# Kernel optimization log

Measured on AMD Instinct MI355X. Metric: run time of the kernel, lower is better.

Reference implementation:

```python
import jax, jax.numpy as jnp
import numpy as np

K = 9            # LCN box-filter size
EPS = 1e-6


def _box_sum(x):
    """9x9 box sum with zero padding 4, separable. x: [N,H,W] -> [N,H,W]."""
    xp = x[:, None]                                  # N,1,H,W
    kh = jnp.ones((1, 1, K, 1), x.dtype)
    kw = jnp.ones((1, 1, 1, K), x.dtype)
    y = jax.lax.conv_general_dilated(xp, kh, (1, 1), [(K // 2, K // 2), (0, 0)])
    y = jax.lax.conv_general_dilated(y, kw, (1, 1), [(0, 0), (K // 2, K // 2)])
    return y[:, 0]


def _lcn(img):
    """Faithful to torch: conv weight is ones(3,3,9,9)/81, i.e. the 'mean' SUMS over
    the 3 input channels of per-pixel 9x9 box means; every output channel is identical.
    So compute channel-sum once, box-filter it, and broadcast back over channels."""
    kk = float(K * K)
    mean_local = _box_sum(img.sum(axis=1)) / kk                 # N,H,W
    mean_sq_local = _box_sum((img * img).sum(axis=1)) / kk      # N,H,W
    std_local = (mean_sq_local - mean_local * mean_local) * kk / (kk - 1.0)
    m = mean_local[:, None]                                     # N,1,H,W (broadcasts over C)
    s = std_local[:, None]
    return (img - m) / (s + EPS), m, s


def _warp(right, disp):
    """Equivalent of affine_grid(identity) + grid -= (disp*2/W, 0) + grid_sample
    (bilinear, zeros padding, align_corners=False). Since the y-coordinate is the
    identity grid, iy == row index exactly, so sampling reduces to 1-D horizontal
    bilinear interpolation at source column ix = j - disp[n,i,j]."""
    N, C, H, W = right.shape
    ix = jnp.arange(W, dtype=right.dtype)[None, None, :] - disp   # N,H,W
    x0 = jnp.floor(ix)
    wx = ix - x0                                                  # frac weight for x1
    x0i = x0.astype(jnp.int32)
    x1i = x0i + 1
    v0 = ((x0i >= 0) & (x0i < W)).astype(right.dtype)             # zeros padding masks
    v1 = ((x1i >= 0) & (x1i < W)).astype(right.dtype)
    i0 = jnp.broadcast_to(jnp.clip(x0i, 0, W - 1)[:, None], right.shape)
    i1 = jnp.broadcast_to(jnp.clip(x1i, 0, W - 1)[:, None], right.shape)
    g0 = jnp.take_along_axis(right, i0, axis=3)                   # N,C,H,W
    g1 = jnp.take_along_axis(right, i1, axis=3)
    return g0 * (v0 * (1.0 - wx))[:, None] + g1 * (v1 * wx)[:, None]


def setup_inputs() -> dict:
    key = jax.random.key(0)
    k1, k2, k3 = jax.random.split(key, 3)
    N, C, H, W = 8, 3, 720, 1280
    left_img = jax.random.uniform(k1, (N, C, H, W), dtype=jnp.float32)
    right_img = jax.random.uniform(k2, (N, C, H, W), dtype=jnp.float32)
    dispmap = jax.random.uniform(k3, (N, H, W), dtype=jnp.float32) * 64.0  # pixels
    return {"left_img": left_img, "right_img": right_img, "dispmap": dispmap}


def reference(left_img, right_img, dispmap):
    recon_img = _warp(right_img, dispmap)
    recon_img_lcn, _, _ = _lcn(recon_img)
    left_img_lcn, _, left_std_local = _lcn(left_img)
    return jnp.abs((left_img_lcn - recon_img_lcn) * left_std_local).mean()
```

## Files before the change

### kernel.cpp

```cpp
#include <hip/hip_runtime.h>

#define NB 8
#define CC 3
#define HH 720
#define WW 1280
#define EPSL 1e-6f
#define HSEG 30
#define NSEG (HH / HSEG)
#define G4   (NSEG / 4)
#define OUTC 56
#define NSTRIP 23
#define NITER (HSEG + 8)
#define NBLK (NB * NSTRIP * G4)

__device__ __forceinline__ float bperm(int addr, float x) {
    return __int_as_float(__builtin_amdgcn_ds_bpermute(addr, __float_as_int(x)));
}

__global__ __launch_bounds__(256)
void fused_loss_kernel(const float* __restrict__ left,
                       const float* __restrict__ right,
                       const float* __restrict__ disp,
                       float* __restrict__ out)
{
    const int t    = threadIdx.x;
    const int lane = t & 63;
    const int wid  = t >> 6;

    const int b     = blockIdx.x;
    const int strip = b % NSTRIP;
    const int g     = (b / NSTRIP) % G4;
    const int n     = b / (NSTRIP * G4);

    const int hseg = g * 4 + wid;
    const int h0   = hseg * HSEG;

    const int gc  = strip * OUTC + lane - 4;
    const int gcc = min(max(gc, 0), WW - 1);
    const float gcf = (float)gc;
    const bool col_ok   = (gc >= 0) && (gc < WW);
    const bool out_lane = (lane >= 4) && (lane < 4 + OUTC) && (gc < WW);

    const size_t plane = (size_t)HH * WW;
    const float* __restrict__ dp  = disp  + (size_t)n * plane;
    const float* __restrict__ lp0 = left  + (size_t)n * CC * plane;
    const float* __restrict__ lp1 = lp0 + plane;
    const float* __restrict__ lp2 = lp1 + plane;
    const float* __restrict__ rp0 = right + (size_t)n * CC * plane;
    const float* __restrict__ rp1 = rp0 + plane;
    const float* __restrict__ rp2 = rp1 + plane;

    const int a_m1 = ((lane + 63) & 63) << 2;
    const int a_p1 = ((lane +  1) & 63) << 2;
    const int a_m3 = ((lane + 61) & 63) << 2;
    const int a_p3 = ((lane +  3) & 63) << 2;

    __shared__ float4 ring[8][256];

    float p1l0=0,p1l1=0,p1l2=0,p1r0=0,p1r1=0,p1r2=0;
    float p2l0=0,p2l1=0,p2l2=0,p2r0=0,p2r1=0,p2r2=0;
    float p3l0=0,p3l1=0,p3l2=0,p3r0=0,p3r1=0,p3r2=0;
    float p4l0=0,p4l1=0,p4l2=0,p4r0=0,p4r1=0,p4r2=0;

    const int r0 = h0 - 4;

    int rcl = min(max(r0, 0), HH - 1);
    unsigned ro = (unsigned)(rcl * WW + gcc);
    float dA  = dp[ro];
    float al0 = lp0[ro], al1 = lp1[ro], al2 = lp2[ro];
    rcl = min(max(r0 + 1, 0), HH - 1);
    unsigned rob = (unsigned)(rcl * WW + gcc);
    float dB  = dp[rob];
    float bl0 = lp0[rob], bl1 = lp1[rob], bl2 = lp2[rob];

    float aw0, aw1, ag00, ag01, ag10, ag11, ag20, ag21;
    {
        float ix  = gcf - dA;
        float x0f = floorf(ix), wx = ix - x0f;
        int x0i = (int)x0f, x1i = x0i + 1;
        float v0 = (x0i >= 0 && x0i < WW) ? 1.f : 0.f;
        float v1 = (x1i >= 0 && x1i < WW) ? 1.f : 0.f;
        int i0 = min(max(x0i, 0), WW - 1), i1 = min(max(x1i, 0), WW - 1);
        aw0 = v0 * (1.f - wx); aw1 = v1 * wx;
        unsigned rb = (unsigned)(min(max(r0, 0), HH - 1) * WW);
        ag00 = rp0[rb + i0]; ag01 = rp0[rb + i1];
        ag10 = rp1[rb + i0]; ag11 = rp1[rb + i1];
        ag20 = rp2[rb + i0]; ag21 = rp2[rb + i1];
    }

    float4 vsum = make_float4(0.f,0.f,0.f,0.f);
    float acc = 0.f;

    for (int iter = 0; iter < NITER; ++iter) {
        const int r = r0 + iter;

        float4 old8 = ring[iter & 7][t];

        int rcl2 = min(max(r + 2, 0), HH - 1);
        unsigned ro2 = (unsigned)(rcl2 * WW + gcc);
        float dC  = dp[ro2];
        float cl0 = lp0[ro2], cl1 = lp1[ro2], cl2 = lp2[ro2];

        float bw0, bw1, bg00, bg01, bg10, bg11, bg20, bg21;
        {
            float ix  = gcf - dB;
            float x0f = floorf(ix), wx = ix - x0f;
            int x0i = (int)x0f, x1i = x0i + 1;
            float v0 = (x0i >= 0 && x0i < WW) ? 1.f : 0.f;
            float v1 = (x1i >= 0 && x1i < WW) ? 1.f : 0.f;
            int i0 = min(max(x0i, 0), WW - 1), i1 = min(max(x1i, 0), WW - 1);
            bw0 = v0 * (1.f - wx); bw1 = v1 * wx;
            unsigned rb = (unsigned)(min(max(r + 1, 0), HH - 1) * WW);
            bg00 = rp0[rb + i0]; bg01 = rp0[rb + i1];
            bg10 = rp1[rb + i0]; bg11 = rp1[rb + i1];
            bg20 = rp2[rb + i0]; bg21 = rp2[rb + i1];
        }

        float rca = ag00*aw0 + ag01*aw1;
        float rcb = ag10*aw0 + ag11*aw1;
        float rcc = ag20*aw0 + ag21*aw1;
        bool valr = col_ok && ((unsigned)r < (unsigned)HH);
        float rx = al0 + al1 + al2;
        float ry = al0*al0 + al1*al1 + al2*al2;
        float rz = rca + rcb + rcc;
        float rw = rca*rca + rcb*rcb + rcc*rcc;
        rx = valr ? rx : 0.f;  ry = valr ? ry : 0.f;
        rz = valr ? rz : 0.f;  rw = valr ? rw : 0.f;

        float sx = bperm(a_m1, rx) + rx + bperm(a_p1, rx);
        float sy = bperm(a_m1, ry) + ry + bperm(a_p1, ry);
        float sz = bperm(a_m1, rz) + rz + bperm(a_p1, rz);
        float sw = bperm(a_m1, rw) + rw + bperm(a_p1, rw);
        float hx = bperm(a_m3, sx) + sx + bperm(a_p3, sx);
        float hy = bperm(a_m3, sy) + sy + bperm(a_p3, sy);
        float hz = bperm(a_m3, sz) + sz + bperm(a_p3, sz);
        float hw = bperm(a_m3, sw) + sw + bperm(a_p3, sw);

        ring[iter & 7][t] = make_float4(hx, hy, hz, hw);

        vsum.x += hx; vsum.y += hy; vsum.z += hz; vsum.w += hw;

        if (iter >= 8) {
            float ml   = vsum.x * (1.f / 81.f);
            float msl  = vsum.y * (1.f / 81.f);
            float stdl = (msl - ml * ml) * (81.f / 80.f);
            float sl   = stdl + EPSL;
            float invl = __builtin_amdgcn_rcpf(sl);
            invl = invl * __builtin_fmaf(-sl, invl, 2.f);
            float mr   = vsum.z * (1.f / 81.f);
            float msr  = vsum.w * (1.f / 81.f);
            float stdr = (msr - mr * mr) * (81.f / 80.f);
            float sr   = stdr + EPSL;
            float invr = __builtin_amdgcn_rcpf(sr);
            invr = invr * __builtin_fmaf(-sr, invr, 2.f);
            if (out_lane) {
                float av, bv;
                av = (p4l0 - ml) * invl; bv = (p4r0 - mr) * invr;
                acc += fabsf((av - bv) * stdl);
                av = (p4l1 - ml) * invl; bv = (p4r1 - mr) * invr;
                acc += fabsf((av - bv) * stdl);
                av = (p4l2 - ml) * invl; bv = (p4r2 - mr) * invr;
                acc += fabsf((av - bv) * stdl);
            }
            vsum.x -= old8.x; vsum.y -= old8.y; vsum.z -= old8.z; vsum.w -= old8.w;
        }

        p4l0=p3l0; p4l1=p3l1; p4l2=p3l2; p4r0=p3r0; p4r1=p3r1; p4r2=p3r2;
        p3l0=p2l0; p3l1=p2l1; p3l2=p2l2; p3r0=p2r0; p3r1=p2r1; p3r2=p2r2;
        p2l0=p1l0; p2l1=p1l1; p2l2=p1l2; p2r0=p1r0; p2r1=p1r1; p2r2=p1r2;
        p1l0=al0;  p1l1=al1;  p1l2=al2;  p1r0=rca;  p1r1=rcb;  p1r2=rcc;

        al0=bl0; al1=bl1; al2=bl2;
        aw0=bw0; aw1=bw1;
        ag00=bg00; ag01=bg01; ag10=bg10; ag11=bg11; ag20=bg20; ag21=bg21;
        dB=dC; bl0=cl0; bl1=cl1; bl2=cl2;
    }

#pragma unroll
    for (int off = 32; off > 0; off >>= 1)
        acc += __shfl_down(acc, off, 64);
    __syncthreads();
    float* red = (float*)&ring[0][0];
    if (lane == 0) red[wid] = acc;
    __syncthreads();
    if (t == 0) {
        float s = red[0] + red[1] + red[2] + red[3];
        const float inv_count = 1.f / ((float)NB * CC * HH * WW);
        atomicAdd(out, s * inv_count);
    }
}

extern "C" void kernel_launch(void* const* d_in, const int* in_sizes, int n_in,
                              void* d_out, int out_size, void* d_ws, size_t ws_size,
                              hipStream_t stream) {
    const float* left  = (const float*)d_in[0];
    const float* right = (const float*)d_in[1];
    const float* disp  = (const float*)d_in[2];
    float* out = (float*)d_out;

    hipMemsetAsync(out, 0, sizeof(float) * out_size, stream);

    hipLaunchKernelGGL(fused_loss_kernel, dim3(NBLK), dim3(256), 0, stream,
                       left, right, disp, out);
}
```

Before: 244.6 us.

## Process two rows per iteration and reload left pixels instead of shifting registers

The row loop now handles two image rows per step, with deeper software prefetch of disparity, left and gathered right values (two rows ahead). The 4-deep register shift chain of left and recon values is replaced: left center pixels are re-read from global memory (likely cached) at output time, and only the recon values are kept in a 2-stage pair chain. The ring buffer is split into two 4-slot rings. The aim is more memory-level parallelism and fewer register moves per row, at the cost of extra global loads, higher register pressure and possible occupancy loss.

```diff
diff --git a/kernel.cpp b/kernel.cpp
--- a/kernel.cpp
+++ b/kernel.cpp
@@ -10,8 +10,45 @@
 #define G4   (NSEG / 4)
 #define OUTC 56
 #define NSTRIP 23
-#define NITER (HSEG + 8)
+#define NST  ((HSEG + 8) / 2)
 #define NBLK (NB * NSTRIP * G4)
+
+#define OFFR(row) ((unsigned)(min(max((row),0),HH-1)*WW + gcc))
+
+#define GATHER(row, dv, w0_, w1_, g00_, g01_, g10_, g11_, g20_, g21_) do { \
+    float ix_ = gcf - (dv); float x0f_ = floorf(ix_); float wx_ = ix_ - x0f_; \
+    int x0i_ = (int)x0f_; int x1i_ = x0i_ + 1;                              \
+    float v0_ = (x0i_ >= 0 && x0i_ < WW) ? 1.f : 0.f;                       \
+    float v1_ = (x1i_ >= 0 && x1i_ < WW) ? 1.f : 0.f;                       \
+    int i0_ = min(max(x0i_,0),WW-1); int i1_ = min(max(x1i_,0),WW-1);       \
+    w0_ = v0_*(1.f-wx_); w1_ = v1_*wx_;                                     \
+    unsigned rb_ = (unsigned)(min(max((row),0),HH-1)*WW);                   \
+    g00_ = rp0[rb_+i0_]; g01_ = rp0[rb_+i1_];                               \
+    g10_ = rp1[rb_+i0_]; g11_ = rp1[rb_+i1_];                               \
+    g20_ = rp2[rb_+i0_]; g21_ = rp2[rb_+i1_]; } while(0)
+
+#define OUTROW(pa,pb,pc, la,lb,lc) do {                                      \
+    float ml_  = vsum.x*(1.f/81.f);                                          \
+    float msl_ = vsum.y*(1.f/81.f);                                          \
+    float stdl_=(msl_-ml_*ml_)*(81.f/80.f);                                  \
+    float sl_=stdl_+EPSL;                                                    \
+    float invl_=__builtin_amdgcn_rcpf(sl_);                                  \
+    invl_ = invl_*__builtin_fmaf(-sl_,invl_,2.f);                            \
+    float mr_  = vsum.z*(1.f/81.f);                                          \
+    float msr_ = vsum.w*(1.f/81.f);                                          \
+    float stdr_=(msr_-mr_*mr_)*(81.f/80.f);                                  \
+    float sr_=stdr_+EPSL;                                                    \
+    float invr_=__builtin_amdgcn_rcpf(sr_);                                  \
+    invr_ = invr_*__builtin_fmaf(-sr_,invr_,2.f);                            \
+    if (out_lane) {                                                          \
+        float av_,bv_;                                                       \
+        av_=((la)-ml_)*invl_; bv_=((pa)-mr_)*invr_;                          \
+        acc += fabsf((av_-bv_)*stdl_);                                       \
+        av_=((lb)-ml_)*invl_; bv_=((pb)-mr_)*invr_;                          \
+        acc += fabsf((av_-bv_)*stdl_);                                       \
+        av_=((lc)-ml_)*invl_; bv_=((pc)-mr_)*invr_;                          \
+        acc += fabsf((av_-bv_)*stdl_);                                       \
+    } } while(0)
 
 __device__ __forceinline__ float bperm(int addr, float x) {
     return __int_as_float(__builtin_amdgcn_ds_bpermute(addr, __float_as_int(x)));
@@ -32,9 +69,7 @@
     const int g     = (b / NSTRIP) % G4;
     const int n     = b / (NSTRIP * G4);
 
-    const int hseg = g * 4 + wid;
-    const int h0   = hseg * HSEG;
-
+    const int h0 = (g * 4 + wid) * HSEG;
     const int gc  = strip * OUTC + lane - 4;
     const int gcc = min(max(gc, 0), WW - 1);
     const float gcf = (float)gc;
@@ -55,132 +90,114 @@
     const int a_m3 = ((lane + 61) & 63) << 2;
     const int a_p3 = ((lane +  3) & 63) << 2;
 
-    __shared__ float4 ring[8][256];
-
-    float p1l0=0,p1l1=0,p1l2=0,p1r0=0,p1r1=0,p1r2=0;
-    float p2l0=0,p2l1=0,p2l2=0,p2r0=0,p2r1=0,p2r2=0;
-    float p3l0=0,p3l1=0,p3l2=0,p3r0=0,p3r1=0,p3r2=0;
-    float p4l0=0,p4l1=0,p4l2=0,p4r0=0,p4r1=0,p4r2=0;
+    __shared__ float4 ringA[4][256];
+    __shared__ float4 ringB[4][256];
 
     const int r0 = h0 - 4;
 
-    int rcl = min(max(r0, 0), HH - 1);
-    unsigned ro = (unsigned)(rcl * WW + gcc);
-    float dA  = dp[ro];
-    float al0 = lp0[ro], al1 = lp1[ro], al2 = lp2[ro];
-    rcl = min(max(r0 + 1, 0), HH - 1);
-    unsigned rob = (unsigned)(rcl * WW + gcc);
-    float dB  = dp[rob];
-    float bl0 = lp0[rob], bl1 = lp1[rob], bl2 = lp2[rob];
-
-    float aw0, aw1, ag00, ag01, ag10, ag11, ag20, ag21;
-    {
-        float ix  = gcf - dA;
-        float x0f = floorf(ix), wx = ix - x0f;
-        int x0i = (int)x0f, x1i = x0i + 1;
-        float v0 = (x0i >= 0 && x0i < WW) ? 1.f : 0.f;
-        float v1 = (x1i >= 0 && x1i < WW) ? 1.f : 0.f;
-        int i0 = min(max(x0i, 0), WW - 1), i1 = min(max(x1i, 0), WW - 1);
-        aw0 = v0 * (1.f - wx); aw1 = v1 * wx;
-        unsigned rb = (unsigned)(min(max(r0, 0), HH - 1) * WW);
-        ag00 = rp0[rb + i0]; ag01 = rp0[rb + i1];
-        ag10 = rp1[rb + i0]; ag11 = rp1[rb + i1];
-        ag20 = rp2[rb + i0]; ag21 = rp2[rb + i1];
-    }
+    unsigned oA0 = OFFR(r0), oA1 = OFFR(r0 + 1);
+    float dA0 = dp[oA0], lA00 = lp0[oA0], lA01 = lp1[oA0], lA02 = lp2[oA0];
+    float dA1 = dp[oA1], lA10 = lp0[oA1], lA11 = lp1[oA1], lA12 = lp2[oA1];
+    unsigned oN0 = OFFR(r0 + 2), oN1 = OFFR(r0 + 3);
+    float dN0 = dp[oN0], lN00 = lp0[oN0], lN01 = lp1[oN0], lN02 = lp2[oN0];
+    float dN1 = dp[oN1], lN10 = lp0[oN1], lN11 = lp1[oN1], lN12 = lp2[oN1];
+    float wA00,wA01, gA00,gA01,gA10,gA11,gA20,gA21;
+    float wA10,wA11, gB00,gB01,gB10,gB11,gB20,gB21;
+    GATHER(r0,     dA0, wA00,wA01, gA00,gA01,gA10,gA11,gA20,gA21);
+    GATHER(r0 + 1, dA1, wA10,wA11, gB00,gB01,gB10,gB11,gB20,gB21);
+
+    float c1a0=0,c1b0=0,c1c0=0, c1a1=0,c1b1=0,c1c1=0;
+    float c2a0=0,c2b0=0,c2c0=0, c2a1=0,c2b1=0,c2c1=0;
 
     float4 vsum = make_float4(0.f,0.f,0.f,0.f);
     float acc = 0.f;
 
-    for (int iter = 0; iter < NITER; ++iter) {
-        const int r = r0 + iter;
-
-        float4 old8 = ring[iter & 7][t];
-
-        int rcl2 = min(max(r + 2, 0), HH - 1);
-        unsigned ro2 = (unsigned)(rcl2 * WW + gcc);
-        float dC  = dp[ro2];
-        float cl0 = lp0[ro2], cl1 = lp1[ro2], cl2 = lp2[ro2];
-
-        float bw0, bw1, bg00, bg01, bg10, bg11, bg20, bg21;
-        {
-            float ix  = gcf - dB;
-            float x0f = floorf(ix), wx = ix - x0f;
-            int x0i = (int)x0f, x1i = x0i + 1;
-            float v0 = (x0i >= 0 && x0i < WW) ? 1.f : 0.f;
-            float v1 = (x1i >= 0 && x1i < WW) ? 1.f : 0.f;
-            int i0 = min(max(x0i, 0), WW - 1), i1 = min(max(x1i, 0), WW - 1);
-            bw0 = v0 * (1.f - wx); bw1 = v1 * wx;
-            unsigned rb = (unsigned)(min(max(r + 1, 0), HH - 1) * WW);
-            bg00 = rp0[rb + i0]; bg01 = rp0[rb + i1];
-            bg10 = rp1[rb + i0]; bg11 = rp1[rb + i1];
-            bg20 = rp2[rb + i0]; bg21 = rp2[rb + i1];
+    for (int k = 0; k < NST; ++k) {
+        const int x0 = r0 + 2*k;
+        const int s  = k & 3;
+
+        float4 old0 = ringA[s][t];
+        float4 old1 = ringB[s][t];
+
+        unsigned oO0 = OFFR(x0 - 4), oO1 = OFFR(x0 - 3);
+        float ol00 = lp0[oO0], ol01 = lp1[oO0], ol02 = lp2[oO0];
+        float ol10 = lp0[oO1], ol11 = lp1[oO1], ol12 = lp2[oO1];
+
+        unsigned oM0 = OFFR(x0 + 4), oM1 = OFFR(x0 + 5);
+        float dM0 = dp[oM0], lM00 = lp0[oM0], lM01 = lp1[oM0], lM02 = lp2[oM0];
+        float dM1 = dp[oM1], lM10 = lp0[oM1], lM11 = lp1[oM1], lM12 = lp2[oM1];
+
+        float wN00,wN01, ng00,ng01,ng10,ng11,ng20,ng21;
+        float wN10,wN11, nh00,nh01,nh10,nh11,nh20,nh21;
+        GATHER(x0 + 2, dN0, wN00,wN01, ng00,ng01,ng10,ng11,ng20,ng21);
+        GATHER(x0 + 3, dN1, wN10,wN11, nh00,nh01,nh10,nh11,nh20,nh21);
+
+        float rca0 = gA00*wA00 + gA01*wA01;
+        float rcb0 = gA10*wA00 + gA11*wA01;
+        float rcc0 = gA20*wA00 + gA21*wA01;
+        float rca1 = gB00*wA10 + gB01*wA11;
+        float rcb1 = gB10*wA10 + gB11*wA11;
+        float rcc1 = gB20*wA10 + gB21*wA11;
+        bool val0 = col_ok && ((unsigned)x0       < (unsigned)HH);
+        bool val1 = col_ok && ((unsigned)(x0 + 1) < (unsigned)HH);
+        float rx0 = lA00+lA01+lA02, ry0 = lA00*lA00+lA01*lA01+lA02*lA02;
+        float rz0 = rca0+rcb0+rcc0, rw0 = rca0*rca0+rcb0*rcb0+rcc0*rcc0;
+        float rx1 = lA10+lA11+lA12, ry1 = lA10*lA10+lA11*lA11+lA12*lA12;
+        float rz1 = rca1+rcb1+rcc1, rw1 = rca1*rca1+rcb1*rcb1+rcc1*rcc1;
+        rx0 = val0 ? rx0 : 0.f; ry0 = val0 ? ry0 : 0.f;
+        rz0 = val0 ? rz0 : 0.f; rw0 = val0 ? rw0 : 0.f;
+        rx1 = val1 ? rx1 : 0.f; ry1 = val1 ? ry1 : 0.f;
+        rz1 = val1 ? rz1 : 0.f; rw1 = val1 ? rw1 : 0.f;
+
+        float sx0 = bperm(a_m1,rx0) + rx0 + bperm(a_p1,rx0);
+        float sy0 = bperm(a_m1,ry0) + ry0 + bperm(a_p1,ry0);
+        float sz0 = bperm(a_m1,rz0) + rz0 + bperm(a_p1,rz0);
+        float sw0 = bperm(a_m1,rw0) + rw0 + bperm(a_p1,rw0);
+        float sx1 = bperm(a_m1,rx1) + rx1 + bperm(a_p1,rx1);
+        float sy1 = bperm(a_m1,ry1) + ry1 + bperm(a_p1,ry1);
+        float sz1 = bperm(a_m1,rz1) + rz1 + bperm(a_p1,rz1);
+        float sw1 = bperm(a_m1,rw1) + rw1 + bperm(a_p1,rw1);
+        float hx0 = bperm(a_m3,sx0) + sx0 + bperm(a_p3,sx0);
+        float hy0 = bperm(a_m3,sy0) + sy0 + bperm(a_p3,sy0);
+        float hz0 = bperm(a_m3,sz0) + sz0 + bperm(a_p3,sz0);
+        float hw0 = bperm(a_m3,sw0) + sw0 + bperm(a_p3,sw0);
+        float hx1 = bperm(a_m3,sx1) + sx1 + bperm(a_p3,sx1);
+        float hy1 = bperm(a_m3,sy1) + sy1 + bperm(a_p3,sy1);
+        float hz1 = bperm(a_m3,sz1) + sz1 + bperm(a_p3,sz1);
+        float hw1 = bperm(a_m3,sw1) + sw1 + bperm(a_p3,sw1);
+
+        float4 h0v = make_float4(hx0,hy0,hz0,hw0);
+        float4 h1v = make_float4(hx1,hy1,hz1,hw1);
+        ringA[s][t] = h0v;
+        ringB[s][t] = h1v;
+
+        vsum.x += h0v.x; vsum.y += h0v.y; vsum.z += h0v.z; vsum.w += h0v.w;
+        if (k >= 4) {
+            OUTROW(c2a0,c2b0,c2c0, ol00,ol01,ol02);
+            vsum.x -= old0.x; vsum.y -= old0.y; vsum.z -= old0.z; vsum.w -= old0.w;
         }
-
-        float rca = ag00*aw0 + ag01*aw1;
-        float rcb = ag10*aw0 + ag11*aw1;
-        float rcc = ag20*aw0 + ag21*aw1;
-        bool valr = col_ok && ((unsigned)r < (unsigned)HH);
-        float rx = al0 + al1 + al2;
-        float ry = al0*al0 + al1*al1 + al2*al2;
-        float rz = rca + rcb + rcc;
-        float rw = rca*rca + rcb*rcb + rcc*rcc;
-        rx = valr ? rx : 0.f;  ry = valr ? ry : 0.f;
-        rz = valr ? rz : 0.f;  rw = valr ? rw : 0.f;
-
-        float sx = bperm(a_m1, rx) + rx + bperm(a_p1, rx);
-        float sy = bperm(a_m1, ry) + ry + bperm(a_p1, ry);
-        float sz = bperm(a_m1, rz) + rz + bperm(a_p1, rz);
-        float sw = bperm(a_m1, rw) + rw + bperm(a_p1, rw);
-        float hx = bperm(a_m3, sx) + sx + bperm(a_p3, sx);
-        float hy = bperm(a_m3, sy) + sy + bperm(a_p3, sy);
-        float hz = bperm(a_m3, sz) + sz + bperm(a_p3, sz);
-        float hw = bperm(a_m3, sw) + sw + bperm(a_p3, sw);
-
-        ring[iter & 7][t] = make_float4(hx, hy, hz, hw);
-
-        vsum.x += hx; vsum.y += hy; vsum.z += hz; vsum.w += hw;
-
-        if (iter >= 8) {
-            float ml   = vsum.x * (1.f / 81.f);
-            float msl  = vsum.y * (1.f / 81.f);
-            float stdl = (msl - ml * ml) * (81.f / 80.f);
-            float sl   = stdl + EPSL;
-            float invl = __builtin_amdgcn_rcpf(sl);
-            invl = invl * __builtin_fmaf(-sl, invl, 2.f);
-            float mr   = vsum.z * (1.f / 81.f);
-            float msr  = vsum.w * (1.f / 81.f);
-            float stdr = (msr - mr * mr) * (81.f / 80.f);
-            float sr   = stdr + EPSL;
-            float invr = __builtin_amdgcn_rcpf(sr);
-            invr = invr * __builtin_fmaf(-sr, invr, 2.f);
-            if (out_lane) {
-                float av, bv;
-                av = (p4l0 - ml) * invl; bv = (p4r0 - mr) * invr;
-                acc += fabsf((av - bv) * stdl);
-                av = (p4l1 - ml) * invl; bv = (p4r1 - mr) * invr;
-                acc += fabsf((av - bv) * stdl);
-                av = (p4l2 - ml) * invl; bv = (p4r2 - mr) * invr;
-                acc += fabsf((av - bv) * stdl);
-            }
-            vsum.x -= old8.x; vsum.y -= old8.y; vsum.z -= old8.z; vsum.w -= old8.w;
+        vsum.x += h1v.x; vsum.y += h1v.y; vsum.z += h1v.z; vsum.w += h1v.w;
+        if (k >= 4) {
+            OUTROW(c2a1,c2b1,c2c1, ol10,ol11,ol12);
+            vsum.x -= old1.x; vsum.y -= old1.y; vsum.z -= old1.z; vsum.w -= old1.w;
         }
 
-        p4l0=p3l0; p4l1=p3l1; p4l2=p3l2; p4r0=p3r0; p4r1=p3r1; p4r2=p3r2;
-        p3l0=p2l0; p3l1=p2l1; p3l2=p2l2; p3r0=p2r0; p3r1=p2r1; p3r2=p2r2;
-        p2l0=p1l0; p2l1=p1l1; p2l2=p1l2; p2r0=p1r0; p2r1=p1r1; p2r2=p1r2;
-        p1l0=al0;  p1l1=al1;  p1l2=al2;  p1r0=rca;  p1r1=rcb;  p1r2=rcc;
-
-        al0=bl0; al1=bl1; al2=bl2;
-        aw0=bw0; aw1=bw1;
-        ag00=bg00; ag01=bg01; ag10=bg10; ag11=bg11; ag20=bg20; ag21=bg21;
-        dB=dC; bl0=cl0; bl1=cl1; bl2=cl2;
+        c2a0=c1a0; c2b0=c1b0; c2c0=c1c0; c2a1=c1a1; c2b1=c1b1; c2c1=c1c1;
+        c1a0=rca0; c1b0=rcb0; c1c0=rcc0; c1a1=rca1; c1b1=rcb1; c1c1=rcc1;
+
+        lA00=lN00; lA01=lN01; lA02=lN02; lA10=lN10; lA11=lN11; lA12=lN12;
+        wA00=wN00; wA01=wN01; wA10=wN10; wA11=wN11;
+        gA00=ng00; gA01=ng01; gA10=ng10; gA11=ng11; gA20=ng20; gA21=ng21;
+        gB00=nh00; gB01=nh01; gB10=nh10; gB11=nh11; gB20=nh20; gB21=nh21;
+        dN0=dM0; lN00=lM00; lN01=lM01; lN02=lM02;
+        dN1=dM1; lN10=lM10; lN11=lM11; lN12=lM12;
     }
 
 #pragma unroll
     for (int off = 32; off > 0; off >>= 1)
         acc += __shfl_down(acc, off, 64);
     __syncthreads();
-    float* red = (float*)&ring[0][0];
+    float* red = (float*)&ringA[0][0];
     if (lane == 0) red[wid] = acc;
     __syncthreads();
     if (t == 0) {
```

Result: slower. 257.5 us (+5.3%).
